# Optimization experiments

Measured on AMD Instinct MI355X. Metric: run time of the kernel, lower is better.

The kernel has to match this reference:

```python
import jax, jax.numpy as jnp
import numpy as np

B, C_IN, H, W = 8, 1024, 18, 80
FEAT = 1024
A = 32      # anchors per location
NCLS = 3    # classes
NREG = 13
K = 3       # kernel size
K2 = K * K
EPS = 1e-5  # BatchNorm eps


def conv2d(x, w, b):
    y = jax.lax.conv_general_dilated(x, w, (1, 1), ((1, 1), (1, 1)),
                                     dimension_numbers=('NCHW', 'OIHW', 'NCHW'))
    return y + b[None, :, None, None]


def bn_eval(x, g, b):
    # eval-mode BatchNorm2d with running_mean=0, running_var=1
    return x * (g / jnp.sqrt(1.0 + EPS))[None, :, None, None] + b[None, :, None, None]


def anchor_flatten(x, d):
    # [B, A*d, H, W] -> permute(0,2,3,1) -> [B, H*W*A, d]
    Bx, Cx, Hx, Wx = x.shape
    return jnp.transpose(x, (0, 2, 3, 1)).reshape(Bx, Hx * Wx * (Cx // d), d)


def bilinear_gather(x, py, px):
    # x: [B,C,H,W]; py/px: [B,K2,H,W] float coords -> [B,C,K2,H,W], zero outside
    Bx, Cx, Hx, Wx = x.shape
    y0 = jnp.floor(py); x0 = jnp.floor(px)
    wy1 = py - y0; wx1 = px - x0
    wy0 = 1.0 - wy1; wx0 = 1.0 - wx1
    xf = x.reshape(Bx, Cx, Hx * Wx)

    def g(yy, xx):
        valid = ((yy >= 0) & (yy < Hx) & (xx >= 0) & (xx < Wx)).astype(x.dtype)
        yc = jnp.clip(yy, 0, Hx - 1).astype(jnp.int32)
        xc = jnp.clip(xx, 0, Wx - 1).astype(jnp.int32)
        idx = (yc * Wx + xc).reshape(Bx, -1)
        vals = jax.vmap(lambda xi, ii: xi[:, ii])(xf, idx).reshape(Bx, Cx, K2, Hx, Wx)
        return vals * valid[:, None]

    return (g(y0, x0) * (wy0 * wx0)[:, None] + g(y0, x0 + 1) * (wy0 * wx1)[:, None]
            + g(y0 + 1, x0) * (wy1 * wx0)[:, None] + g(y0 + 1, x0 + 1) * (wy1 * wx1)[:, None])


def mdcn(x, off_w, off_b, w, b):
    # ModulatedDeformConvPack (DCNv2): 3x3 conv -> (dy, dx, mask), then modulated deform conv
    out = conv2d(x, off_w, off_b)                        # [B, 3*K2, H, W]
    dy, dx, m = out[:, :K2], out[:, K2:2 * K2], jax.nn.sigmoid(out[:, 2 * K2:])
    ky, kx = jnp.meshgrid(jnp.arange(K, dtype=x.dtype), jnp.arange(K, dtype=x.dtype), indexing='ij')
    base_y = jnp.arange(x.shape[2], dtype=x.dtype)[None, None, :, None] - 1.0 + ky.reshape(1, K2, 1, 1)
    base_x = jnp.arange(x.shape[3], dtype=x.dtype)[None, None, None, :] - 1.0 + kx.reshape(1, K2, 1, 1)
    sampled = bilinear_gather(x, base_y + dy, base_x + dx) * m[:, None]   # [B,C,K2,H,W]
    O = w.shape[0]
    return jnp.einsum('bckhw,ock->bohw', sampled, w.reshape(O, w.shape[1], K2)) + b[None, :, None, None]


def setup_inputs() -> dict:
    key = jax.random.key(0)
    ks = jax.random.split(key, 10)
    s1 = 1.0 / np.sqrt(C_IN * K2)
    s2 = 1.0 / np.sqrt(FEAT * K2)
    rn = lambda k, sh, sc: jax.random.normal(k, sh, jnp.float32) * sc
    return {
        'features': jax.random.normal(ks[0], (B, C_IN, H, W), jnp.float32),
        'cls_w1': rn(ks[1], (FEAT, C_IN, K, K), s1), 'cls_b1': jnp.zeros((FEAT,), jnp.float32),
        'cls_w2': rn(ks[2], (FEAT, FEAT, K, K), s2), 'cls_b2': jnp.zeros((FEAT,), jnp.float32),
        'cls_w3': rn(ks[3], (A * NCLS, FEAT, K, K), s2), 'cls_b3': jnp.zeros((A * NCLS,), jnp.float32),
        'off_w': rn(ks[4], (3 * K2, C_IN, K, K), s1), 'off_b': jnp.zeros((3 * K2,), jnp.float32),
        'dcn_w': rn(ks[5], (FEAT, C_IN, K, K), s1), 'dcn_b': jnp.zeros((FEAT,), jnp.float32),
        'bn1_g': jnp.ones((FEAT,), jnp.float32), 'bn1_b': jnp.zeros((FEAT,), jnp.float32),
        'reg_w2': rn(ks[6], (FEAT, FEAT, K, K), s2), 'reg_b2': jnp.zeros((FEAT,), jnp.float32),
        'bn2_g': jnp.ones((FEAT,), jnp.float32), 'bn2_b': jnp.zeros((FEAT,), jnp.float32),
        'reg_w3': rn(ks[7], (A * NREG, FEAT, K, K), s2), 'reg_b3': jnp.zeros((A * NREG,), jnp.float32),
    }


def reference(features, cls_w1, cls_b1, cls_w2, cls_b2, cls_w3, cls_b3,
              off_w, off_b, dcn_w, dcn_b, bn1_g, bn1_b,
              reg_w2, reg_b2, bn2_g, bn2_b, reg_w3, reg_b3):
    # cls branch (Dropout2d is identity in eval)
    h = jax.nn.relu(conv2d(features, cls_w1, cls_b1))
    h = jax.nn.relu(conv2d(h, cls_w2, cls_b2))
    cls_preds = anchor_flatten(conv2d(h, cls_w3, cls_b3), NCLS)   # [B, H*W*A, NCLS]
    # reg branch: modulated deformable conv -> BN -> ReLU -> conv -> BN -> ReLU -> conv
    r = jax.nn.relu(bn_eval(mdcn(features, off_w, off_b, dcn_w, dcn_b), bn1_g, bn1_b))
    r = jax.nn.relu(bn_eval(conv2d(r, reg_w2, reg_b2), bn2_g, bn2_b))
    reg_preds = anchor_flatten(conv2d(r, reg_w3, reg_b3), NREG)   # [B, H*W*A, NREG]
    return (cls_preds, reg_preds)
```

## Files before the change

### kernel.cpp

```cpp
#include <hip/hip_runtime.h>
#include <math.h>

typedef short short8 __attribute__((ext_vector_type(8)));
typedef float f32x4 __attribute__((ext_vector_type(4)));
typedef unsigned short u16;
typedef unsigned int u32;

#define GAS(p) ((__attribute__((address_space(1))) void*)(p))
#define LAS(p) ((__attribute__((address_space(3))) void*)(p))

namespace {

constexpr int HW   = 1440;
constexpr int PBAT = 20 * 82 * 1024;

__device__ __forceinline__ u16 f2bf(float f) {
  u32 u = __float_as_uint(f);
  u32 r = (u + 0x7FFFu + ((u >> 16) & 1u)) >> 16;
  return (u16)r;
}
__device__ __forceinline__ float bf2f(u16 h) {
  return __uint_as_float(((u32)h) << 16);
}

__global__ __launch_bounds__(256)
void transpose_feat(const float* __restrict__ src, u16* __restrict__ dst) {
  __shared__ float tile[128][17];
  const int bh = blockIdx.y;
  const int b = bh / 18, h = bh % 18;
  const int wt = blockIdx.x % 5, ct = blockIdx.x / 5;
  const int w0 = wt * 16, c0 = ct * 128;
  const int tid = threadIdx.x;
#pragma unroll
  for (int it = 0; it < 8; ++it) {
    int idx = it * 256 + tid;
    int c = idx >> 4, w = idx & 15;
    tile[c][w] = src[((size_t)(b * 1024 + c0 + c) * 18 + h) * 80 + w0 + w];
  }
  __syncthreads();
  const int px = tid >> 4, cq = tid & 15;
  union { uint4 u; u16 s[8]; } pk;
#pragma unroll
  for (int j = 0; j < 8; ++j) pk.s[j] = f2bf(tile[cq * 8 + j][px]);
  *(uint4*)(dst + ((size_t)(b * 20 + h + 1) * 82 + (w0 + px + 1)) * 1024 + c0 + cq * 8) = pk.u;
}

__global__ __launch_bounds__(256)
void repack_w(const float* __restrict__ src, u16* __restrict__ dst, int O) {
  int idx = blockIdx.x * 256 + threadIdx.x;
  if (idx >= O * 128) return;
  int o = idx >> 7, c8 = idx & 127;
  const float* s = src + (size_t)o * 9216 + (size_t)c8 * 72;
  float v[72];
#pragma unroll
  for (int i = 0; i < 18; ++i) {
    float4 f = *(const float4*)(s + i * 4);
    v[i * 4 + 0] = f.x; v[i * 4 + 1] = f.y; v[i * 4 + 2] = f.z; v[i * 4 + 3] = f.w;
  }
#pragma unroll
  for (int t = 0; t < 9; ++t) {
    union { uint4 u; u16 h[8]; } pk;
#pragma unroll
    for (int j = 0; j < 8; ++j) pk.h[j] = f2bf(v[j * 9 + t]);
    *(uint4*)(dst + ((size_t)t * O + o) * 1024 + c8 * 8) = pk.u;
  }
}

__global__ __launch_bounds__(256)
void sample_k(const u16* __restrict__ featP, const float* __restrict__ offp,
              u16* __restrict__ spl, int pix0, int Npc) {
  const int tid = threadIdx.x;
  const int k = blockIdx.y;
  const int lp = blockIdx.x * 16 + (tid >> 4);
  const int p = pix0 + lp;
  const int c8 = tid & 15;
  int b = p / HW, hw = p - b * HW;
  int h = hw / 80, w = hw - h * 80;
  float dy = offp[p * 27 + k];
  float dx = offp[p * 27 + 9 + k];
  float ml = offp[p * 27 + 18 + k];
  float m = 1.f / (1.f + expf(-ml));
  float py = (float)(h - 1 + k / 3) + dy;
  float px = (float)(w - 1 + (k % 3)) + dx;
  float y0f = floorf(py), x0f = floorf(px);
  float wy1 = py - y0f, wx1 = px - x0f;
  float wy0 = 1.f - wy1, wx0 = 1.f - wx1;
  int y0 = (int)y0f, x0 = (int)x0f;
  int ya = min(max(y0, -1), 18),  yb = min(max(y0 + 1, -1), 18);
  int xa = min(max(x0, -1), 80),  xb = min(max(x0 + 1, -1), 80);
  const u16* base = featP + (size_t)b * PBAT;
  const u16* r00 = base + ((size_t)(ya + 1) * 82 + (xa + 1)) * 1024;
  const u16* r01 = base + ((size_t)(ya + 1) * 82 + (xb + 1)) * 1024;
  const u16* r10 = base + ((size_t)(yb + 1) * 82 + (xa + 1)) * 1024;
  const u16* r11 = base + ((size_t)(yb + 1) * 82 + (xb + 1)) * 1024;
  float w00 = wy0 * wx0 * m, w01 = wy0 * wx1 * m;
  float w10 = wy1 * wx0 * m, w11 = wy1 * wx1 * m;
  u16* dst = spl + ((size_t)k * Npc + lp) * 1024;
  for (int c = c8 * 8; c < 1024; c += 128) {
    union { uint4 u; u16 h[8]; } a, bq, cq2, d, o;
    a.u   = *(const uint4*)(r00 + c);
    bq.u  = *(const uint4*)(r01 + c);
    cq2.u = *(const uint4*)(r10 + c);
    d.u   = *(const uint4*)(r11 + c);
#pragma unroll
    for (int j = 0; j < 8; ++j) {
      float v = w00 * bf2f(a.h[j]) + w01 * bf2f(bq.h[j]) +
                w10 * bf2f(cq2.h[j]) + w11 * bf2f(d.h[j]);
      o.h[j] = f2bf(v);
    }
    *(uint4*)(dst + c) = o.u;
  }
}

template<int PLANES, int STOREF32, int HASBN, int HASRELU>
__global__ __launch_bounds__(256)
void mfma_conv(const u16* __restrict__ W, const u16* __restrict__ Bp,
               const float* __restrict__ bias, const float* __restrict__ bng,
               const float* __restrict__ bnb, void* __restrict__ outv,
               int Co, int pix0, int Npc) {
  __shared__ __align__(16) u16 As[128 * 32];
  __shared__ __align__(16) u16 Bs[128 * 32];
  const int tid = threadIdx.x;
  const int wv = tid >> 6, lane = tid & 63;
  const int o0 = blockIdx.y * 128;
  const int p0 = pix0 + blockIdx.x * 128;

  const int lr = lane >> 2;
  const int qs = (lane & 3) ^ ((lane >> 3) & 3);
  int aoff[2], boff[2];
#pragma unroll
  for (int s = 0; s < 2; ++s) {
    int r = (wv * 2 + s) * 16 + lr;
    int o = min(o0 + r, Co - 1);
    aoff[s] = o * 1024 + qs * 8;
    int p = p0 + r;
    if (PLANES) {
      boff[s] = (p - pix0) * 1024 + qs * 8;
    } else {
      int b = p / HW, hw = p - b * HW;
      int h = hw / 80, w = hw - h * 80;
      boff[s] = ((b * 20 + h) * 82 + w) * 1024 + qs * 8;
    }
  }
  u16* aDst = As + (wv * 2) * 512;
  u16* bDst = Bs + (wv * 2) * 512;

  const int wm = wv >> 1, wn = wv & 1;
  const int frm = lane & 15;
  const int kq = lane >> 4;
  const int sel = (kq ^ ((lane >> 1) & 3)) * 16;

  f32x4 acc[4][4];
#pragma unroll
  for (int i = 0; i < 4; ++i)
#pragma unroll
    for (int j = 0; j < 4; ++j) acc[i][j] = (f32x4)0.f;

  for (int t = 0; t < 9; ++t) {
    const u16* Wt = W + (size_t)t * Co * 1024;
    const u16* Bt = Bp + (PLANES ? (size_t)t * (size_t)Npc * 1024
                                 : (size_t)(((t / 3) * 82 + (t % 3)) * 1024));
    for (int cc = 0; cc < 1024; cc += 32) {
      __syncthreads();
#pragma unroll
      for (int s = 0; s < 2; ++s) {
        __builtin_amdgcn_global_load_lds(GAS(Wt + aoff[s] + cc), LAS(aDst + s * 512), 16, 0, 0);
        __builtin_amdgcn_global_load_lds(GAS(Bt + boff[s] + cc), LAS(bDst + s * 512), 16, 0, 0);
      }
      __syncthreads();
      uint4 af[4], bf4[4];
#pragma unroll
      for (int i = 0; i < 4; ++i) {
        af[i]  = *(const uint4*)((const char*)As + (wm * 64 + i * 16 + frm) * 64 + sel);
        bf4[i] = *(const uint4*)((const char*)Bs + (wn * 64 + i * 16 + frm) * 64 + sel);
      }
#pragma unroll
      for (int i = 0; i < 4; ++i) {
        short8 a = __builtin_bit_cast(short8, af[i]);
#pragma unroll
        for (int j = 0; j < 4; ++j) {
          short8 b = __builtin_bit_cast(short8, bf4[j]);
          acc[i][j] = __builtin_amdgcn_mfma_f32_16x16x32_bf16(a, b, acc[i][j], 0, 0, 0);
        }
      }
    }
  }

  size_t obase[4];
#pragma unroll
  for (int j = 0; j < 4; ++j) {
    int pn = p0 + wn * 64 + j * 16 + frm;
    if (STOREF32) {
      obase[j] = (size_t)pn * Co;
    } else {
      int b = pn / HW, hw = pn - b * HW;
      int h = hw / 80, w = hw - h * 80;
      obase[j] = ((size_t)(b * 20 + h + 1) * 82 + (w + 1)) * 1024;
    }
  }
#pragma unroll
  for (int i = 0; i < 4; ++i) {
    int o = o0 + wm * 64 + i * 16 + kq * 4;
    float bi[4], sc[4], sh[4];
#pragma unroll
    for (int r = 0; r < 4; ++r) {
      int oc = min(o + r, Co - 1);
      bi[r] = bias[oc];
      if (HASBN) { sc[r] = bng[oc] * rsqrtf(1.f + 1e-5f); sh[r] = bnb[oc]; }
    }
#pragma unroll
    for (int j = 0; j < 4; ++j) {
      float v[4];
#pragma unroll
      for (int r = 0; r < 4; ++r) {
        float x = acc[i][j][r] + bi[r];
        if (HASBN) x = x * sc[r] + sh[r];
        if (HASRELU) x = fmaxf(x, 0.f);
        v[r] = x;
      }
      if (STOREF32) {
        float* op = (float*)outv;
#pragma unroll
        for (int r = 0; r < 4; ++r)
          if (o + r < Co) op[obase[j] + o + r] = v[r];
      } else {
        u16* op = (u16*)outv;
        union { ulonglong1 dummy; } ;
        ushort4 pk;
        pk.x = f2bf(v[0]); pk.y = f2bf(v[1]); pk.z = f2bf(v[2]); pk.w = f2bf(v[3]);
        *(ushort4*)(op + obase[j] + o) = pk;
      }
    }
  }
}

}

extern "C" void kernel_launch(void* const* d_in, const int* in_sizes, int n_in,
                              void* d_out, int out_size, void* d_ws, size_t ws_size,
                              hipStream_t stream) {
  const float* feat   = (const float*)d_in[0];
  const float* cls_w1 = (const float*)d_in[1];
  const float* cls_b1 = (const float*)d_in[2];
  const float* cls_w2 = (const float*)d_in[3];
  const float* cls_b2 = (const float*)d_in[4];
  const float* cls_w3 = (const float*)d_in[5];
  const float* cls_b3 = (const float*)d_in[6];
  const float* off_w  = (const float*)d_in[7];
  const float* off_b  = (const float*)d_in[8];
  const float* dcn_w  = (const float*)d_in[9];
  const float* dcn_b  = (const float*)d_in[10];
  const float* bn1_g  = (const float*)d_in[11];
  const float* bn1_b  = (const float*)d_in[12];
  const float* reg_w2 = (const float*)d_in[13];
  const float* reg_b2 = (const float*)d_in[14];
  const float* bn2_g  = (const float*)d_in[15];
  const float* bn2_b  = (const float*)d_in[16];
  const float* reg_w3 = (const float*)d_in[17];
  const float* reg_b3 = (const float*)d_in[18];
  float* outp = (float*)d_out;

  const size_t ACTB = 26869760;
  char* wsb = (char*)d_ws;
  u16* featP = (u16*)(wsb);
  u16* actA  = (u16*)(wsb + ACTB);
  u16* actB  = (u16*)(wsb + 2 * ACTB);
  u16* wts   = (u16*)(wsb + 3 * ACTB);
  float* offp = (float*)(wsb + 3 * ACTB + 85432320);
  u16* spl   = (u16*)(wsb + 3 * ACTB + 85432320 + 1244160);
  const size_t BASE = 3 * ACTB + 85432320 + 1244160;

  u16* offT = wts;
  u16* w1T  = wts + 248832;
  u16* w2T  = wts + 9686016;
  u16* w3T  = wts + 19123200;
  u16* dcnT = wts + 20007936;
  u16* r2T  = wts + 29445120;
  u16* r3T  = wts + 38882304;

  size_t avail = ws_size > BASE ? ws_size - BASE : 0;
  int tiles = (int)(avail / 2359296);
  if (tiles < 1) tiles = 1;
  if (tiles > 90) tiles = 90;

  dim3 blk(256);

  hipMemsetAsync(featP, 0, ACTB, stream);
  hipMemsetAsync(actA, 0, ACTB, stream);
  hipMemsetAsync(actB, 0, ACTB, stream);

  transpose_feat<<<dim3(40, 144), blk, 0, stream>>>(feat, featP);

  repack_w<<<dim3(14),  blk, 0, stream>>>(off_w,  offT, 27);
  repack_w<<<dim3(512), blk, 0, stream>>>(cls_w1, w1T, 1024);
  repack_w<<<dim3(512), blk, 0, stream>>>(cls_w2, w2T, 1024);
  repack_w<<<dim3(48),  blk, 0, stream>>>(cls_w3, w3T, 96);
  repack_w<<<dim3(512), blk, 0, stream>>>(dcn_w,  dcnT, 1024);
  repack_w<<<dim3(512), blk, 0, stream>>>(reg_w2, r2T, 1024);
  repack_w<<<dim3(208), blk, 0, stream>>>(reg_w3, r3T, 416);

  mfma_conv<0, 1, 0, 0><<<dim3(90, 1), blk, 0, stream>>>(
      offT, featP, off_b, nullptr, nullptr, offp, 27, 0, 0);

  for (int t0 = 0; t0 < 90; t0 += tiles) {
    int nt = (90 - t0) < tiles ? (90 - t0) : tiles;
    int pix0 = t0 * 128, np = nt * 128;
    sample_k<<<dim3(nt * 8, 9), blk, 0, stream>>>(featP, offp, spl, pix0, np);
    mfma_conv<1, 0, 1, 1><<<dim3(nt, 8), blk, 0, stream>>>(
        dcnT, spl, dcn_b, bn1_g, bn1_b, actB, 1024, pix0, np);
  }

  mfma_conv<0, 0, 0, 1><<<dim3(90, 8), blk, 0, stream>>>(
      w1T, featP, cls_b1, nullptr, nullptr, actA, 1024, 0, 0);
  mfma_conv<0, 0, 0, 1><<<dim3(90, 8), blk, 0, stream>>>(
      w2T, actA, cls_b2, nullptr, nullptr, featP, 1024, 0, 0);
  mfma_conv<0, 1, 0, 0><<<dim3(90, 1), blk, 0, stream>>>(
      w3T, featP, cls_b3, nullptr, nullptr, outp, 96, 0, 0);

  mfma_conv<0, 0, 1, 1><<<dim3(90, 8), blk, 0, stream>>>(
      r2T, actB, reg_b2, bn2_g, bn2_b, actA, 1024, 0, 0);
  mfma_conv<0, 1, 0, 0><<<dim3(90, 4), blk, 0, stream>>>(
      r3T, actA, reg_b3, nullptr, nullptr, outp + 1105920, 416, 0, 0);
}
```

Before: 2.232 ms.

## Merge independent convs and sampling into shared launches to fill the GPU

Collapses the seven weight-repack launches into one segmented kernel and merges the three memsets into one. Independent GEMMs now share a launch through a runtime-flag gemm body: cls1 with the offset conv, cls2 with the deformable sampling, and the DCN conv with cls3. When the workspace is large enough, the tiled sample/DCN loop becomes a single pass. This cuts launch count and fills the GPU with blocks from several jobs, but replaces compile-time template flags with runtime branches, which may cost registers or code quality in the hot GEMM.

```diff
diff --git a/kernel.cpp b/kernel.cpp
--- a/kernel.cpp
+++ b/kernel.cpp
@@ -16,8 +16,7 @@
 
 __device__ __forceinline__ u16 f2bf(float f) {
   u32 u = __float_as_uint(f);
-  u32 r = (u + 0x7FFFu + ((u >> 16) & 1u)) >> 16;
-  return (u16)r;
+  return (u16)((u + 0x7FFFu + ((u >> 16) & 1u)) >> 16);
 }
 __device__ __forceinline__ float bf2f(u16 h) {
   return __uint_as_float(((u32)h) << 16);
@@ -45,9 +44,25 @@
   *(uint4*)(dst + ((size_t)(b * 20 + h + 1) * 82 + (w0 + px + 1)) * 1024 + c0 + cq * 8) = pk.u;
 }
 
-__global__ __launch_bounds__(256)
-void repack_w(const float* __restrict__ src, u16* __restrict__ dst, int O) {
-  int idx = blockIdx.x * 256 + threadIdx.x;
+struct RepackArgs {
+  const float* src[7];
+  u16* dst[7];
+  int O[7];
+  int start[7];
+  int nseg;
+};
+
+__global__ __launch_bounds__(256)
+void repack_all(RepackArgs ra) {
+  int blk = blockIdx.x;
+  int seg = 0;
+#pragma unroll
+  for (int i = 1; i < 7; ++i)
+    if (i < ra.nseg && blk >= ra.start[i]) seg = i;
+  const float* src = ra.src[seg];
+  u16* dst = ra.dst[seg];
+  const int O = ra.O[seg];
+  int idx = (blk - ra.start[seg]) * 256 + threadIdx.x;
   if (idx >= O * 128) return;
   int o = idx >> 7, c8 = idx & 127;
   const float* s = src + (size_t)o * 9216 + (size_t)c8 * 72;
@@ -66,12 +81,10 @@
   }
 }
 
-__global__ __launch_bounds__(256)
-void sample_k(const u16* __restrict__ featP, const float* __restrict__ offp,
-              u16* __restrict__ spl, int pix0, int Npc) {
-  const int tid = threadIdx.x;
-  const int k = blockIdx.y;
-  const int lp = blockIdx.x * 16 + (tid >> 4);
+__device__ __forceinline__
+void sample_body(int k, int lp, int pix0, int Npc,
+                 const u16* __restrict__ featP, const float* __restrict__ offp,
+                 u16* __restrict__ spl, int tid) {
   const int p = pix0 + lp;
   const int c8 = tid & 15;
   int b = p / HW, hw = p - b * HW;
@@ -112,18 +125,27 @@
   }
 }
 
-template<int PLANES, int STOREF32, int HASBN, int HASRELU>
-__global__ __launch_bounds__(256)
-void mfma_conv(const u16* __restrict__ W, const u16* __restrict__ Bp,
-               const float* __restrict__ bias, const float* __restrict__ bng,
-               const float* __restrict__ bnb, void* __restrict__ outv,
-               int Co, int pix0, int Npc) {
+__global__ __launch_bounds__(256)
+void sample_standalone(const u16* __restrict__ featP, const float* __restrict__ offp,
+                       u16* __restrict__ spl, int pix0, int Npc) {
+  sample_body(blockIdx.y, blockIdx.x * 16 + (threadIdx.x >> 4), pix0, Npc,
+              featP, offp, spl, threadIdx.x);
+}
+
+struct Job {
+  const u16* W; const u16* B;
+  const float* bias; const float* bng; const float* bnb;
+  void* out; int Co; int flags; int pix0; int Npc;
+};
+
+__device__ void gemm_body(const Job J, int px, int oy) {
   __shared__ __align__(16) u16 As[128 * 32];
   __shared__ __align__(16) u16 Bs[128 * 32];
   const int tid = threadIdx.x;
   const int wv = tid >> 6, lane = tid & 63;
-  const int o0 = blockIdx.y * 128;
-  const int p0 = pix0 + blockIdx.x * 128;
+  const int o0 = oy * 128;
+  const int p0 = J.pix0 + px * 128;
+  const bool planes = J.flags & 1;
 
   const int lr = lane >> 2;
   const int qs = (lane & 3) ^ ((lane >> 3) & 3);
@@ -131,11 +153,11 @@
 #pragma unroll
   for (int s = 0; s < 2; ++s) {
     int r = (wv * 2 + s) * 16 + lr;
-    int o = min(o0 + r, Co - 1);
+    int o = min(o0 + r, J.Co - 1);
     aoff[s] = o * 1024 + qs * 8;
     int p = p0 + r;
-    if (PLANES) {
-      boff[s] = (p - pix0) * 1024 + qs * 8;
+    if (planes) {
+      boff[s] = (p - J.pix0) * 1024 + qs * 8;
     } else {
       int b = p / HW, hw = p - b * HW;
       int h = hw / 80, w = hw - h * 80;
@@ -157,9 +179,9 @@
     for (int j = 0; j < 4; ++j) acc[i][j] = (f32x4)0.f;
 
   for (int t = 0; t < 9; ++t) {
-    const u16* Wt = W + (size_t)t * Co * 1024;
-    const u16* Bt = Bp + (PLANES ? (size_t)t * (size_t)Npc * 1024
-                                 : (size_t)(((t / 3) * 82 + (t % 3)) * 1024));
+    const u16* Wt = J.W + (size_t)t * J.Co * 1024;
+    const u16* Bt = J.B + (planes ? (size_t)t * (size_t)J.Npc * 1024
+                                  : (size_t)(((t / 3) * 82 + (t % 3)) * 1024));
     for (int cc = 0; cc < 1024; cc += 32) {
       __syncthreads();
 #pragma unroll
@@ -186,12 +208,15 @@
     }
   }
 
+  const bool f32out = J.flags & 2;
+  const bool hasbn  = J.flags & 4;
+  const bool hasrelu= J.flags & 8;
   size_t obase[4];
 #pragma unroll
   for (int j = 0; j < 4; ++j) {
     int pn = p0 + wn * 64 + j * 16 + frm;
-    if (STOREF32) {
-      obase[j] = (size_t)pn * Co;
+    if (f32out) {
+      obase[j] = (size_t)pn * J.Co;
     } else {
       int b = pn / HW, hw = pn - b * HW;
       int h = hw / 80, w = hw - h * 80;
@@ -204,9 +229,10 @@
     float bi[4], sc[4], sh[4];
 #pragma unroll
     for (int r = 0; r < 4; ++r) {
-      int oc = min(o + r, Co - 1);
-      bi[r] = bias[oc];
-      if (HASBN) { sc[r] = bng[oc] * rsqrtf(1.f + 1e-5f); sh[r] = bnb[oc]; }
+      int oc = min(o + r, J.Co - 1);
+      bi[r] = J.bias[oc];
+      if (hasbn) { sc[r] = J.bng[oc] * rsqrtf(1.f + 1e-5f); sh[r] = J.bnb[oc]; }
+      else { sc[r] = 1.f; sh[r] = 0.f; }
     }
 #pragma unroll
     for (int j = 0; j < 4; ++j) {
@@ -214,23 +240,42 @@
 #pragma unroll
       for (int r = 0; r < 4; ++r) {
         float x = acc[i][j][r] + bi[r];
-        if (HASBN) x = x * sc[r] + sh[r];
-        if (HASRELU) x = fmaxf(x, 0.f);
+        if (hasbn) x = x * sc[r] + sh[r];
+        if (hasrelu) x = fmaxf(x, 0.f);
         v[r] = x;
       }
-      if (STOREF32) {
-        float* op = (float*)outv;
+      if (f32out) {
+        float* op = (float*)J.out;
 #pragma unroll
         for (int r = 0; r < 4; ++r)
-          if (o + r < Co) op[obase[j] + o + r] = v[r];
+          if (o + r < J.Co) op[obase[j] + o + r] = v[r];
       } else {
-        u16* op = (u16*)outv;
-        union { ulonglong1 dummy; } ;
+        u16* op = (u16*)J.out;
         ushort4 pk;
         pk.x = f2bf(v[0]); pk.y = f2bf(v[1]); pk.z = f2bf(v[2]); pk.w = f2bf(v[3]);
         *(ushort4*)(op + obase[j] + o) = pk;
       }
     }
+  }
+}
+
+__global__ __launch_bounds__(256)
+void gemm_dual(Job j0, Job j1, int ysplit) {
+  int y = blockIdx.y;
+  if (y < ysplit) gemm_body(j0, blockIdx.x, y);
+  else            gemm_body(j1, blockIdx.x, y - ysplit);
+}
+
+__global__ __launch_bounds__(256)
+void gemm_sample(Job j, const u16* __restrict__ featP, const float* __restrict__ offp,
+                 u16* __restrict__ spl, int gemmBlocks) {
+  int gx = blockIdx.x;
+  if (gx < gemmBlocks) {
+    gemm_body(j, gx % 90, gx / 90);
+  } else {
+    int sidx = gx - gemmBlocks;
+    int k = sidx / 720, bs = sidx % 720;
+    sample_body(k, bs * 16 + (threadIdx.x >> 4), 0, 11520, featP, offp, spl, threadIdx.x);
   }
 }
 
@@ -263,12 +308,13 @@
   const size_t ACTB = 26869760;
   char* wsb = (char*)d_ws;
   u16* featP = (u16*)(wsb);
-  u16* actA  = (u16*)(wsb + ACTB);
-  u16* actB  = (u16*)(wsb + 2 * ACTB);
+  u16* bufA  = (u16*)(wsb + ACTB);
+  u16* bufB  = (u16*)(wsb + 2 * ACTB);
   u16* wts   = (u16*)(wsb + 3 * ACTB);
   float* offp = (float*)(wsb + 3 * ACTB + 85432320);
   u16* spl   = (u16*)(wsb + 3 * ACTB + 85432320 + 1244160);
   const size_t BASE = 3 * ACTB + 85432320 + 1244160;
+  const size_t SPLB = (size_t)9 * 11520 * 1024 * 2;
 
   u16* offT = wts;
   u16* w1T  = wts + 248832;
@@ -278,47 +324,54 @@
   u16* r2T  = wts + 29445120;
   u16* r3T  = wts + 38882304;
 
-  size_t avail = ws_size > BASE ? ws_size - BASE : 0;
-  int tiles = (int)(avail / 2359296);
-  if (tiles < 1) tiles = 1;
-  if (tiles > 90) tiles = 90;
-
   dim3 blk(256);
 
-  hipMemsetAsync(featP, 0, ACTB, stream);
-  hipMemsetAsync(actA, 0, ACTB, stream);
-  hipMemsetAsync(actB, 0, ACTB, stream);
-
+  hipMemsetAsync(featP, 0, 3 * ACTB, stream);
   transpose_feat<<<dim3(40, 144), blk, 0, stream>>>(feat, featP);
 
-  repack_w<<<dim3(14),  blk, 0, stream>>>(off_w,  offT, 27);
-  repack_w<<<dim3(512), blk, 0, stream>>>(cls_w1, w1T, 1024);
-  repack_w<<<dim3(512), blk, 0, stream>>>(cls_w2, w2T, 1024);
-  repack_w<<<dim3(48),  blk, 0, stream>>>(cls_w3, w3T, 96);
-  repack_w<<<dim3(512), blk, 0, stream>>>(dcn_w,  dcnT, 1024);
-  repack_w<<<dim3(512), blk, 0, stream>>>(reg_w2, r2T, 1024);
-  repack_w<<<dim3(208), blk, 0, stream>>>(reg_w3, r3T, 416);
-
-  mfma_conv<0, 1, 0, 0><<<dim3(90, 1), blk, 0, stream>>>(
-      offT, featP, off_b, nullptr, nullptr, offp, 27, 0, 0);
-
-  for (int t0 = 0; t0 < 90; t0 += tiles) {
-    int nt = (90 - t0) < tiles ? (90 - t0) : tiles;
-    int pix0 = t0 * 128, np = nt * 128;
-    sample_k<<<dim3(nt * 8, 9), blk, 0, stream>>>(featP, offp, spl, pix0, np);
-    mfma_conv<1, 0, 1, 1><<<dim3(nt, 8), blk, 0, stream>>>(
-        dcnT, spl, dcn_b, bn1_g, bn1_b, actB, 1024, pix0, np);
-  }
-
-  mfma_conv<0, 0, 0, 1><<<dim3(90, 8), blk, 0, stream>>>(
-      w1T, featP, cls_b1, nullptr, nullptr, actA, 1024, 0, 0);
-  mfma_conv<0, 0, 0, 1><<<dim3(90, 8), blk, 0, stream>>>(
-      w2T, actA, cls_b2, nullptr, nullptr, featP, 1024, 0, 0);
-  mfma_conv<0, 1, 0, 0><<<dim3(90, 1), blk, 0, stream>>>(
-      w3T, featP, cls_b3, nullptr, nullptr, outp, 96, 0, 0);
-
-  mfma_conv<0, 0, 1, 1><<<dim3(90, 8), blk, 0, stream>>>(
-      r2T, actB, reg_b2, bn2_g, bn2_b, actA, 1024, 0, 0);
-  mfma_conv<0, 1, 0, 0><<<dim3(90, 4), blk, 0, stream>>>(
-      r3T, actA, reg_b3, nullptr, nullptr, outp + 1105920, 416, 0, 0);
-}
+  {
+    RepackArgs ra;
+    const float* s[7] = {off_w, cls_w1, cls_w2, cls_w3, dcn_w, reg_w2, reg_w3};
+    u16* d[7] = {offT, w1T, w2T, w3T, dcnT, r2T, r3T};
+    int  O[7] = {27, 1024, 1024, 96, 1024, 1024, 416};
+    int acc = 0;
+    for (int i = 0; i < 7; ++i) {
+      ra.src[i] = s[i]; ra.dst[i] = d[i]; ra.O[i] = O[i]; ra.start[i] = acc;
+      acc += (O[i] * 128 + 255) / 256;
+    }
+    ra.nseg = 7;
+    repack_all<<<dim3(acc), blk, 0, stream>>>(ra);
+  }
+
+  Job jOff  = {offT, featP, off_b, nullptr, nullptr, offp, 27, 2, 0, 0};
+  Job jCls1 = {w1T, featP, cls_b1, nullptr, nullptr, bufA, 1024, 8, 0, 0};
+  Job jCls2 = {w2T, bufA, cls_b2, nullptr, nullptr, bufB, 1024, 8, 0, 0};
+  Job jCls3 = {w3T, bufB, cls_b3, nullptr, nullptr, outp, 96, 2, 0, 0};
+  Job jReg2 = {r2T, bufA, reg_b2, bn2_g, bn2_b, bufB, 1024, 4 | 8, 0, 0};
+  Job jReg3 = {r3T, bufB, reg_b3, nullptr, nullptr, outp + 1105920, 416, 2, 0, 0};
+
+  gemm_dual<<<dim3(90, 9), blk, 0, stream>>>(jCls1, jOff, 8);
+
+  if (ws_size >= BASE + SPLB) {
+    gemm_sample<<<dim3(720 + 6480), blk, 0, stream>>>(jCls2, featP, offp, spl, 720);
+    Job jDcn = {dcnT, spl, dcn_b, bn1_g, bn1_b, bufA, 1024, 1 | 4 | 8, 0, 11520};
+    gemm_dual<<<dim3(90, 9), blk, 0, stream>>>(jDcn, jCls3, 8);
+  } else {
+    gemm_dual<<<dim3(90, 8), blk, 0, stream>>>(jCls2, jCls2, 8);
+    size_t avail = ws_size > BASE ? ws_size - BASE : 0;
+    int tiles = (int)(avail / 2359296);
+    if (tiles < 1) tiles = 1;
+    if (tiles > 90) tiles = 90;
+    for (int t0 = 0; t0 < 90; t0 += tiles) {
+      int nt = (90 - t0) < tiles ? (90 - t0) : tiles;
+      int pix0 = t0 * 128, np = nt * 128;
+      sample_standalone<<<dim3(nt * 8, 9), blk, 0, stream>>>(featP, offp, spl, pix0, np);
+      Job jDcn = {dcnT, spl, dcn_b, bn1_g, bn1_b, bufA, 1024, 1 | 4 | 8, pix0, np};
+      gemm_dual<<<dim3(nt, 8), blk, 0, stream>>>(jDcn, jDcn, 8);
+    }
+    gemm_dual<<<dim3(90, 1), blk, 0, stream>>>(jCls3, jCls3, 1);
+  }
+
+  gemm_dual<<<dim3(90, 8), blk, 0, stream>>>(jReg2, jReg2, 8);
+  gemm_dual<<<dim3(90, 4), blk, 0, stream>>>(jReg3, jReg3, 4);
+}
```

Result: slower. 3.505 ms (+57.0%).

## Co-schedule deformable sampling with cls conv GEMM and batch weight repacks

Applied to the files above, without the earlier changes.

Adds a combined kernel that runs the second cls-branch 3x3 conv GEMM and, in extra blocks of the same grid, the full-batch deformable bilinear sampling. The two independent stages can then share the GPU instead of running back to back, and the tiled sample/conv loop becomes a single full-batch launch. The seven weight-repack launches are merged into one segmented launch, and the three memsets into one. The fast path only runs when the workspace can hold the full sampled buffer; otherwise the old tiled path remains. It also shuffles buffer assignments, which adds some risk of aliasing mistakes.

```diff
diff --git a/kernel.cpp b/kernel.cpp
--- a/kernel.cpp
+++ b/kernel.cpp
@@ -16,8 +16,7 @@
 
 __device__ __forceinline__ u16 f2bf(float f) {
   u32 u = __float_as_uint(f);
-  u32 r = (u + 0x7FFFu + ((u >> 16) & 1u)) >> 16;
-  return (u16)r;
+  return (u16)((u + 0x7FFFu + ((u >> 16) & 1u)) >> 16);
 }
 __device__ __forceinline__ float bf2f(u16 h) {
   return __uint_as_float(((u32)h) << 16);
@@ -45,9 +44,25 @@
   *(uint4*)(dst + ((size_t)(b * 20 + h + 1) * 82 + (w0 + px + 1)) * 1024 + c0 + cq * 8) = pk.u;
 }
 
+struct RepackArgs {
+  const float* src[7];
+  u16* dst[7];
+  int O[7];
+  int start[7];
+  int nseg;
+};
+
 __global__ __launch_bounds__(256)
-void repack_w(const float* __restrict__ src, u16* __restrict__ dst, int O) {
-  int idx = blockIdx.x * 256 + threadIdx.x;
+void repack_all(RepackArgs ra) {
+  int blk = blockIdx.x;
+  int seg = 0;
+#pragma unroll
+  for (int i = 1; i < 7; ++i)
+    if (i < ra.nseg && blk >= ra.start[i]) seg = i;
+  const float* src = ra.src[seg];
+  u16* dst = ra.dst[seg];
+  const int O = ra.O[seg];
+  int idx = (blk - ra.start[seg]) * 256 + threadIdx.x;
   if (idx >= O * 128) return;
   int o = idx >> 7, c8 = idx & 127;
   const float* s = src + (size_t)o * 9216 + (size_t)c8 * 72;
@@ -66,12 +81,10 @@
   }
 }
 
-__global__ __launch_bounds__(256)
-void sample_k(const u16* __restrict__ featP, const float* __restrict__ offp,
-              u16* __restrict__ spl, int pix0, int Npc) {
-  const int tid = threadIdx.x;
-  const int k = blockIdx.y;
-  const int lp = blockIdx.x * 16 + (tid >> 4);
+__device__ __forceinline__
+void sample_body(int k, int lp, int pix0, int Npc,
+                 const u16* __restrict__ featP, const float* __restrict__ offp,
+                 u16* __restrict__ spl, int tid) {
   const int p = pix0 + lp;
   const int c8 = tid & 15;
   int b = p / HW, hw = p - b * HW;
@@ -112,6 +125,13 @@
   }
 }
 
+__global__ __launch_bounds__(256)
+void sample_standalone(const u16* __restrict__ featP, const float* __restrict__ offp,
+                       u16* __restrict__ spl, int pix0, int Npc) {
+  sample_body(blockIdx.y, blockIdx.x * 16 + (threadIdx.x >> 4), pix0, Npc,
+              featP, offp, spl, threadIdx.x);
+}
+
 template<int PLANES, int STOREF32, int HASBN, int HASRELU>
 __global__ __launch_bounds__(256)
 void mfma_conv(const u16* __restrict__ W, const u16* __restrict__ Bp,
@@ -225,11 +245,112 @@
           if (o + r < Co) op[obase[j] + o + r] = v[r];
       } else {
         u16* op = (u16*)outv;
-        union { ulonglong1 dummy; } ;
         ushort4 pk;
         pk.x = f2bf(v[0]); pk.y = f2bf(v[1]); pk.z = f2bf(v[2]); pk.w = f2bf(v[3]);
         *(ushort4*)(op + obase[j] + o) = pk;
       }
+    }
+  }
+}
+
+__global__ __launch_bounds__(256)
+void gemm_sample(const u16* __restrict__ W, const u16* __restrict__ Bp,
+                 const float* __restrict__ bias, void* __restrict__ outv, int Co,
+                 const u16* __restrict__ featP, const float* __restrict__ offp,
+                 u16* __restrict__ spl, int gemmBlocks) {
+  __shared__ __align__(16) u16 As[128 * 32];
+  __shared__ __align__(16) u16 Bs[128 * 32];
+  const int gx = blockIdx.x;
+  const int tid = threadIdx.x;
+  if (gx >= gemmBlocks) {
+    int sidx = gx - gemmBlocks;
+    int k = sidx / 720, bs = sidx % 720;
+    sample_body(k, bs * 16 + (tid >> 4), 0, 11520, featP, offp, spl, tid);
+    return;
+  }
+  const int wv = tid >> 6, lane = tid & 63;
+  const int o0 = (gx / 90) * 128;
+  const int p0 = (gx % 90) * 128;
+
+  const int lr = lane >> 2;
+  const int qs = (lane & 3) ^ ((lane >> 3) & 3);
+  int aoff[2], boff[2];
+#pragma unroll
+  for (int s = 0; s < 2; ++s) {
+    int r = (wv * 2 + s) * 16 + lr;
+    int o = min(o0 + r, Co - 1);
+    aoff[s] = o * 1024 + qs * 8;
+    int p = p0 + r;
+    int b = p / HW, hw = p - b * HW;
+    int h = hw / 80, w = hw - h * 80;
+    boff[s] = ((b * 20 + h) * 82 + w) * 1024 + qs * 8;
+  }
+  u16* aDst = As + (wv * 2) * 512;
+  u16* bDst = Bs + (wv * 2) * 512;
+
+  const int wm = wv >> 1, wn = wv & 1;
+  const int frm = lane & 15;
+  const int kq = lane >> 4;
+  const int sel = (kq ^ ((lane >> 1) & 3)) * 16;
+
+  f32x4 acc[4][4];
+#pragma unroll
+  for (int i = 0; i < 4; ++i)
+#pragma unroll
+    for (int j = 0; j < 4; ++j) acc[i][j] = (f32x4)0.f;
+
+  for (int t = 0; t < 9; ++t) {
+    const u16* Wt = W + (size_t)t * Co * 1024;
+    const u16* Bt = Bp + (size_t)(((t / 3) * 82 + (t % 3)) * 1024);
+    for (int cc = 0; cc < 1024; cc += 32) {
+      __syncthreads();
+#pragma unroll
+      for (int s = 0; s < 2; ++s) {
+        __builtin_amdgcn_global_load_lds(GAS(Wt + aoff[s] + cc), LAS(aDst + s * 512), 16, 0, 0);
+        __builtin_amdgcn_global_load_lds(GAS(Bt + boff[s] + cc), LAS(bDst + s * 512), 16, 0, 0);
+      }
+      __syncthreads();
+      uint4 af[4], bf4[4];
+#pragma unroll
+      for (int i = 0; i < 4; ++i) {
+        af[i]  = *(const uint4*)((const char*)As + (wm * 64 + i * 16 + frm) * 64 + sel);
+        bf4[i] = *(const uint4*)((const char*)Bs + (wn * 64 + i * 16 + frm) * 64 + sel);
+      }
+#pragma unroll
+      for (int i = 0; i < 4; ++i) {
+        short8 a = __builtin_bit_cast(short8, af[i]);
+#pragma unroll
+        for (int j = 0; j < 4; ++j) {
+          short8 b = __builtin_bit_cast(short8, bf4[j]);
+          acc[i][j] = __builtin_amdgcn_mfma_f32_16x16x32_bf16(a, b, acc[i][j], 0, 0, 0);
+        }
+      }
+    }
+  }
+
+  size_t obase[4];
+#pragma unroll
+  for (int j = 0; j < 4; ++j) {
+    int pn = p0 + wn * 64 + j * 16 + frm;
+    int b = pn / HW, hw = pn - b * HW;
+    int h = hw / 80, w = hw - h * 80;
+    obase[j] = ((size_t)(b * 20 + h + 1) * 82 + (w + 1)) * 1024;
+  }
+#pragma unroll
+  for (int i = 0; i < 4; ++i) {
+    int o = o0 + wm * 64 + i * 16 + kq * 4;
+    float bi[4];
+#pragma unroll
+    for (int r = 0; r < 4; ++r) bi[r] = bias[min(o + r, Co - 1)];
+#pragma unroll
+    for (int j = 0; j < 4; ++j) {
+      u16* op = (u16*)outv;
+      ushort4 pk;
+      pk.x = f2bf(fmaxf(acc[i][j][0] + bi[0], 0.f));
+      pk.y = f2bf(fmaxf(acc[i][j][1] + bi[1], 0.f));
+      pk.z = f2bf(fmaxf(acc[i][j][2] + bi[2], 0.f));
+      pk.w = f2bf(fmaxf(acc[i][j][3] + bi[3], 0.f));
+      *(ushort4*)(op + obase[j] + o) = pk;
     }
   }
 }
@@ -263,12 +384,13 @@
   const size_t ACTB = 26869760;
   char* wsb = (char*)d_ws;
   u16* featP = (u16*)(wsb);
-  u16* actA  = (u16*)(wsb + ACTB);
-  u16* actB  = (u16*)(wsb + 2 * ACTB);
+  u16* bufA  = (u16*)(wsb + ACTB);
+  u16* bufB  = (u16*)(wsb + 2 * ACTB);
   u16* wts   = (u16*)(wsb + 3 * ACTB);
   float* offp = (float*)(wsb + 3 * ACTB + 85432320);
   u16* spl   = (u16*)(wsb + 3 * ACTB + 85432320 + 1244160);
   const size_t BASE = 3 * ACTB + 85432320 + 1244160;
+  const size_t SPLB = (size_t)9 * 11520 * 1024 * 2;
 
   u16* offT = wts;
   u16* w1T  = wts + 248832;
@@ -278,47 +400,61 @@
   u16* r2T  = wts + 29445120;
   u16* r3T  = wts + 38882304;
 
-  size_t avail = ws_size > BASE ? ws_size - BASE : 0;
-  int tiles = (int)(avail / 2359296);
-  if (tiles < 1) tiles = 1;
-  if (tiles > 90) tiles = 90;
-
   dim3 blk(256);
 
-  hipMemsetAsync(featP, 0, ACTB, stream);
-  hipMemsetAsync(actA, 0, ACTB, stream);
-  hipMemsetAsync(actB, 0, ACTB, stream);
-
+  hipMemsetAsync(featP, 0, 3 * ACTB, stream);
   transpose_feat<<<dim3(40, 144), blk, 0, stream>>>(feat, featP);
 
-  repack_w<<<dim3(14),  blk, 0, stream>>>(off_w,  offT, 27);
-  repack_w<<<dim3(512), blk, 0, stream>>>(cls_w1, w1T, 1024);
-  repack_w<<<dim3(512), blk, 0, stream>>>(cls_w2, w2T, 1024);
-  repack_w<<<dim3(48),  blk, 0, stream>>>(cls_w3, w3T, 96);
-  repack_w<<<dim3(512), blk, 0, stream>>>(dcn_w,  dcnT, 1024);
-  repack_w<<<dim3(512), blk, 0, stream>>>(reg_w2, r2T, 1024);
-  repack_w<<<dim3(208), blk, 0, stream>>>(reg_w3, r3T, 416);
+  {
+    RepackArgs ra;
+    const float* s[7] = {off_w, cls_w1, cls_w2, cls_w3, dcn_w, reg_w2, reg_w3};
+    u16* d[7] = {offT, w1T, w2T, w3T, dcnT, r2T, r3T};
+    int  O[7] = {27, 1024, 1024, 96, 1024, 1024, 416};
+    int acc = 0;
+    for (int i = 0; i < 7; ++i) {
+      ra.src[i] = s[i]; ra.dst[i] = d[i]; ra.O[i] = O[i]; ra.start[i] = acc;
+      acc += (O[i] * 128 + 255) / 256;
+    }
+    ra.nseg = 7;
+    repack_all<<<dim3(acc), blk, 0, stream>>>(ra);
+  }
 
   mfma_conv<0, 1, 0, 0><<<dim3(90, 1), blk, 0, stream>>>(
       offT, featP, off_b, nullptr, nullptr, offp, 27, 0, 0);
 
-  for (int t0 = 0; t0 < 90; t0 += tiles) {
-    int nt = (90 - t0) < tiles ? (90 - t0) : tiles;
-    int pix0 = t0 * 128, np = nt * 128;
-    sample_k<<<dim3(nt * 8, 9), blk, 0, stream>>>(featP, offp, spl, pix0, np);
-    mfma_conv<1, 0, 1, 1><<<dim3(nt, 8), blk, 0, stream>>>(
-        dcnT, spl, dcn_b, bn1_g, bn1_b, actB, 1024, pix0, np);
-  }
-
   mfma_conv<0, 0, 0, 1><<<dim3(90, 8), blk, 0, stream>>>(
-      w1T, featP, cls_b1, nullptr, nullptr, actA, 1024, 0, 0);
-  mfma_conv<0, 0, 0, 1><<<dim3(90, 8), blk, 0, stream>>>(
-      w2T, actA, cls_b2, nullptr, nullptr, featP, 1024, 0, 0);
-  mfma_conv<0, 1, 0, 0><<<dim3(90, 1), blk, 0, stream>>>(
-      w3T, featP, cls_b3, nullptr, nullptr, outp, 96, 0, 0);
-
-  mfma_conv<0, 0, 1, 1><<<dim3(90, 8), blk, 0, stream>>>(
-      r2T, actB, reg_b2, bn2_g, bn2_b, actA, 1024, 0, 0);
-  mfma_conv<0, 1, 0, 0><<<dim3(90, 4), blk, 0, stream>>>(
-      r3T, actA, reg_b3, nullptr, nullptr, outp + 1105920, 416, 0, 0);
-}
+      w1T, featP, cls_b1, nullptr, nullptr, bufA, 1024, 0, 0);
+
+  if (ws_size >= BASE + SPLB) {
+    gemm_sample<<<dim3(720 + 6480), blk, 0, stream>>>(
+        w2T, bufA, cls_b2, bufB, 1024, featP, offp, spl, 720);
+    mfma_conv<1, 0, 1, 1><<<dim3(90, 8), blk, 0, stream>>>(
+        dcnT, spl, dcn_b, bn1_g, bn1_b, featP, 1024, 0, 11520);
+    mfma_conv<0, 1, 0, 0><<<dim3(90, 1), blk, 0, stream>>>(
+        w3T, bufB, cls_b3, nullptr, nullptr, outp, 96, 0, 0);
+    mfma_conv<0, 0, 1, 1><<<dim3(90, 8), blk, 0, stream>>>(
+        r2T, featP, reg_b2, bn2_g, bn2_b, bufA, 1024, 0, 0);
+    mfma_conv<0, 1, 0, 0><<<dim3(90, 4), blk, 0, stream>>>(
+        r3T, bufA, reg_b3, nullptr, nullptr, outp + 1105920, 416, 0, 0);
+  } else {
+    mfma_conv<0, 0, 0, 1><<<dim3(90, 8), blk, 0, stream>>>(
+        w2T, bufA, cls_b2, nullptr, nullptr, bufB, 1024, 0, 0);
+    size_t avail = ws_size > BASE ? ws_size - BASE : 0;
+    int tiles = (int)(avail / 2359296);
+    if (tiles < 1) tiles = 1;
+    if (tiles > 90) tiles = 90;
+    for (int t0 = 0; t0 < 90; t0 += tiles) {
+      int nt = (90 - t0) < tiles ? (90 - t0) : tiles;
+      int pix0 = t0 * 128, np = nt * 128;
+      sample_standalone<<<dim3(nt * 8, 9), blk, 0, stream>>>(featP, offp, spl, pix0, np);
+      mfma_conv<1, 0, 1, 1><<<dim3(nt, 8), blk, 0, stream>>>(
+          dcnT, spl, dcn_b, bn1_g, bn1_b, bufA, 1024, pix0, np);
+    }
+    mfma_conv<0, 1, 0, 0><<<dim3(90, 1), blk, 0, stream>>>(
+        w3T, bufB, cls_b3, nullptr, nullptr, outp, 96, 0, 0);
+    mfma_conv<0, 0, 1, 1><<<dim3(90, 8), blk, 0, stream>>>(
+        r2T, bufA, reg_b2, bn2_g, bn2_b, featP, 1024, 0, 0);
+    mfma_conv<0, 1, 0, 0><<<dim3(90, 4), blk, 0, stream>>>(
+        r3T, featP, reg_b3, nullptr, nullptr, outp + 1105920, 416, 0, 0);
+  }
+}
```

Result: faster. 2.185 ms (-2.1%).
